# Optimization experiments

Hardware: AMD Instinct MI355X
Metric: run time of the kernel (lower is better)

The kernel has to match this reference:

```python
import jax, jax.numpy as jnp
import numpy as np

N = 131072      # total nodes = num_graphs * numNodes
E = 2097152     # edges (avg degree 16)
C_IN = 64
HID = 64        # hiddenChannels
NODES = 128     # numNodes per graph
B = 1024        # num_graphs
NCLS = 4


def setup_inputs() -> dict:
    key = jax.random.key(0)
    ks = jax.random.split(key, 10)
    x = jax.random.normal(ks[0], (N, C_IN), jnp.float32)
    edge_index = jax.random.randint(ks[1], (2, E), 0, N, dtype=jnp.int32)
    edge_attr = jax.random.uniform(ks[2], (E,), jnp.float32)
    # GCNConv params (stored as [in, out]); PyG uses glorot init, bias zeros
    W1 = jax.random.normal(ks[3], (C_IN, 2 * HID), jnp.float32) * (1.0 / np.sqrt(C_IN))
    b1 = jnp.zeros((2 * HID,), jnp.float32)
    W2 = jax.random.normal(ks[4], (2 * HID, HID), jnp.float32) * (1.0 / np.sqrt(2 * HID))
    b2 = jnp.zeros((HID,), jnp.float32)
    Wfc = jax.random.normal(ks[5], (HID * NODES, NCLS), jnp.float32) * (1.0 / np.sqrt(HID * NODES))
    bfc = jnp.zeros((NCLS,), jnp.float32)
    return {"x": x, "edge_index": edge_index, "edge_attr": edge_attr,
            "W1": W1, "b1": b1, "W2": W2, "b2": b2, "Wfc": Wfc, "bfc": bfc}


def gcn_conv(x, src, dst, ew, W, b):
    # PyG GCNConv: add self-loops (weight 1), symmetric normalization,
    # linear transform, scatter-add aggregation at target nodes, + bias.
    loop = jnp.arange(N, dtype=src.dtype)
    s = jnp.concatenate([src, loop])
    d = jnp.concatenate([dst, loop])
    w = jnp.concatenate([ew, jnp.ones((N,), ew.dtype)])
    deg = jax.ops.segment_sum(w, d, num_segments=N)                  # [N]
    dis = jnp.where(deg > 0, jax.lax.rsqrt(jnp.maximum(deg, 1e-30)), 0.0)
    norm = dis[s] * w * dis[d]                                       # [E+N]
    h = x @ W                                                        # [N, out]
    msg = h[s] * norm[:, None]                                       # gather + scale
    out = jax.ops.segment_sum(msg, d, num_segments=N)                # scatter-add
    return out + b


def reference(x, edge_index, edge_attr, W1, b1, W2, b2, Wfc, bfc):
    src, dst = edge_index[0], edge_index[1]
    h = jax.nn.relu(gcn_conv(x, src, dst, edge_attr, W1, b1))
    h = jax.nn.relu(gcn_conv(h, src, dst, edge_attr, W2, b2))
    h = h.reshape(B, HID * NODES)
    logits = h @ Wfc + bfc
    return jax.nn.softmax(logits, axis=1)
```

## Files before the change

kernel.cpp:

```cpp
#include <hip/hip_runtime.h>

#define N_NODES 131072
#define NE      2097152
#define CIN     64
#define HID     64
#define H2X     128
#define NODESG  128
#define NGRAPH  1024
#define NCLS    4

#define NBUCK   256
#define NPB     512
#define HBLK    1024
#define EPB     2048
#define DEGSC   1048576.0f
#define DEGMASK ((1ull << 40) - 1)

typedef short bf16x8 __attribute__((ext_vector_type(8)));
typedef float f32x4  __attribute__((ext_vector_type(4)));

__device__ __forceinline__ unsigned short f2b(float f) {
    unsigned int u = __float_as_uint(f);
    return (unsigned short)((u + 0x7fffu + ((u >> 16) & 1u)) >> 16);
}
__device__ __forceinline__ unsigned int pack2(float a, float b) {
    return (unsigned int)f2b(a) | ((unsigned int)f2b(b) << 16);
}
__device__ __forceinline__ float blo(unsigned u) { return __uint_as_float(u << 16); }
__device__ __forceinline__ float bhi(unsigned u) { return __uint_as_float(u & 0xffff0000u); }


__global__ __launch_bounds__(256) void k_wswiz(
        const float* __restrict__ W1, const float* __restrict__ W2,
        unsigned short* __restrict__ wf1, unsigned short* __restrict__ wf2) {
    int tid = threadIdx.x;
    #pragma unroll
    for (int it = 0; it < 4; ++it) {
        int idx = tid + 256 * it;
        int kt = idx >> 9, nt = (idx >> 6) & 7, l = idx & 63;
        int lm = l & 15, lq = l >> 4;
        unsigned pk[4];
        #pragma unroll
        for (int jp = 0; jp < 4; ++jp) {
            float w0 = W1[(kt*32 + lq*8 + 2*jp)     * H2X + nt*16 + lm];
            float w1 = W1[(kt*32 + lq*8 + 2*jp + 1) * H2X + nt*16 + lm];
            pk[jp] = pack2(w0, w1);
        }
        *(uint4*)&wf1[idx * 8] = make_uint4(pk[0], pk[1], pk[2], pk[3]);
    }
    #pragma unroll
    for (int it = 0; it < 4; ++it) {
        int idx = tid + 256 * it;
        int kt = idx >> 8, nt = (idx >> 6) & 3, l = idx & 63;
        int lm = l & 15, lq = l >> 4;
        unsigned pk[4];
        #pragma unroll
        for (int jp = 0; jp < 4; ++jp) {
            float w0 = W2[(kt*32 + lq*8 + 2*jp)     * HID + nt*16 + lm];
            float w1 = W2[(kt*32 + lq*8 + 2*jp + 1) * HID + nt*16 + lm];
            pk[jp] = pack2(w0, w1);
        }
        *(uint4*)&wf2[idx * 8] = make_uint4(pk[0], pk[1], pk[2], pk[3]);
    }
}


__global__ __launch_bounds__(256) void k_hist(const int* __restrict__ dst,
                                              int* __restrict__ hist) {
    __shared__ unsigned bh[NBUCK];
    int t = threadIdx.x;
    bh[t] = 0;
    __syncthreads();
    int base = blockIdx.x * EPB;
    #pragma unroll
    for (int k = 0; k < EPB / 256; ++k) {
        int d = dst[base + t + 256 * k];
        atomicAdd(&bh[d >> 9], 1u);
    }
    __syncthreads();
    hist[t * HBLK + blockIdx.x] = (int)bh[t];
}

__global__ void k_scan1(const int* __restrict__ in, int* __restrict__ out,
                        int* __restrict__ partial) {
    __shared__ int sd[256];
    int t = threadIdx.x;
    int base = blockIdx.x * 512;
    int c0 = in[base + 2*t];
    int c1 = in[base + 2*t + 1];
    int loc = c0 + c1;
    sd[t] = loc;
    __syncthreads();
    for (int off = 1; off < 256; off <<= 1) {
        int v = (t >= off) ? sd[t - off] : 0;
        __syncthreads();
        sd[t] += v;
        __syncthreads();
    }
    int excl = sd[t] - loc;
    out[base + 2*t]     = excl;
    out[base + 2*t + 1] = excl + c0;
    if (t == 255) partial[blockIdx.x] = sd[t];
}

__global__ void k_scan2(int* __restrict__ partial) {
    __shared__ int sd[256];
    int t = threadIdx.x;
    int p0 = partial[2*t], p1 = partial[2*t + 1];
    int loc = p0 + p1;
    sd[t] = loc;
    __syncthreads();
    for (int off = 1; off < 256; off <<= 1) {
        int v = (t >= off) ? sd[t - off] : 0;
        __syncthreads();
        sd[t] += v;
        __syncthreads();
    }
    int excl = sd[t] - loc;
    partial[2*t]     = excl;
    partial[2*t + 1] = excl + p0;
}

__global__ void k_scan3(int* __restrict__ data, const int* __restrict__ partial) {
    int i = blockIdx.x * blockDim.x + threadIdx.x;
    data[i] += partial[i >> 9];
}

__global__ __launch_bounds__(256) void k_scatter(
        const int* __restrict__ src, const int* __restrict__ dst,
        const float* __restrict__ ew, const int* __restrict__ hist,
        unsigned long long* __restrict__ part) {
    __shared__ unsigned lcur[NBUCK];
    int t = threadIdx.x;
    lcur[t] = (unsigned)hist[t * HBLK + blockIdx.x];
    __syncthreads();
    int base = blockIdx.x * EPB;
    #pragma unroll
    for (int k = 0; k < EPB / 256; ++k) {
        int e = base + t + 256 * k;
        int s = src[e], d = dst[e];
        unsigned w = __float_as_uint(ew[e]);
        unsigned p = atomicAdd(&lcur[d >> 9], 1u);
        part[p] = ((unsigned long long)w << 32) |
                  ((unsigned long long)(unsigned)(d & 511) << 17) |
                  (unsigned long long)(unsigned)s;
    }
}

__global__ __launch_bounds__(256) void k_bucket(
        const unsigned long long* __restrict__ part, const int* __restrict__ hist,
        int2* __restrict__ csr, int* __restrict__ rowptr,
        int* __restrict__ counts, float* __restrict__ dis) {
    __shared__ unsigned long long dc[NPB];
    __shared__ unsigned cnt2[NPB];
    __shared__ int rp[NPB];
    __shared__ int sd[256];
    int t = threadIdx.x, b = blockIdx.x;
    dc[t] = 0; dc[t + 256] = 0;
    cnt2[t] = 0; cnt2[t + 256] = 0;
    __syncthreads();
    int start = hist[b * HBLK];
    int end   = (b == NBUCK - 1) ? NE : hist[(b + 1) * HBLK];

    for (int j = start + t; j < end; j += 256) {
        unsigned long long p = part[j];
        unsigned dl = (unsigned)(p >> 17) & 511u;
        float w = __uint_as_float((unsigned)(p >> 32));
        atomicAdd(&dc[dl], (1ull << 40) | (unsigned long long)(unsigned)(w * DEGSC));
    }
    __syncthreads();

    unsigned long long d0 = dc[2*t], d1 = dc[2*t + 1];
    int c0 = (int)(d0 >> 40), c1 = (int)(d1 >> 40);
    int loc = c0 + c1;
    sd[t] = loc;
    __syncthreads();
    for (int off = 1; off < 256; off <<= 1) {
        int v = (t >= off) ? sd[t - off] : 0;
        __syncthreads();
        sd[t] += v;
        __syncthreads();
    }
    int excl = sd[t] - loc;
    rp[2*t] = excl; rp[2*t + 1] = excl + c0;

    int n0 = b * NPB;
    rowptr[n0 + 2*t]     = start + excl;
    rowptr[n0 + 2*t + 1] = start + excl + c0;
    counts[n0 + 2*t]     = c0;
    counts[n0 + 2*t + 1] = c1;
    float dg0 = (float)(d0 & DEGMASK) * (1.0f / DEGSC);
    float dg1 = (float)(d1 & DEGMASK) * (1.0f / DEGSC);
    dis[n0 + 2*t]     = rsqrtf(dg0 + 1.0f);
    dis[n0 + 2*t + 1] = rsqrtf(dg1 + 1.0f);
    __syncthreads();

    for (int j = start + t; j < end; j += 256) {
        unsigned long long p = part[j];
        unsigned dl = (unsigned)(p >> 17) & 511u;
        int s = (int)(p & 0x1ffffu);
        unsigned r = atomicAdd(&cnt2[dl], 1u);
        csr[start + rp[dl] + (int)r] = make_int2(s, (int)(unsigned)(p >> 32));
    }
}

__global__ void k_xcast(const float* __restrict__ x, const float* __restrict__ dis,
                        uint2* __restrict__ xb2) {
    int i = blockIdx.x * blockDim.x + threadIdx.x;
    float d = dis[i >> 4];
    float4 v = ((const float4*)x)[i];
    xb2[i] = make_uint2(pack2(d * v.x, d * v.y), pack2(d * v.z, d * v.w));
}


#define GATHER_PAIR(TAB, pA, pB, nA, nB, cmA, cmB, a0,a1,a2,a3, b0,b1,b2,b3, vSA, vSB) \
    {                                                                                  \
        int   sA0 = __shfl(pA.x, qid),      sA1 = __shfl(pA.x, qid + 4);               \
        int   sA2 = __shfl(pA.x, qid + 8),  sA3 = __shfl(pA.x, qid + 12);              \
        float fA0 = __int_as_float(__shfl(pA.y, qid));                                 \
        float fA1 = __int_as_float(__shfl(pA.y, qid + 4));                             \
        float fA2 = __int_as_float(__shfl(pA.y, qid + 8));                             \
        float fA3 = __int_as_float(__shfl(pA.y, qid + 12));                            \
        int   sB0 = __shfl(pB.x, qid),      sB1 = __shfl(pB.x, qid + 4);               \
        int   sB2 = __shfl(pB.x, qid + 8),  sB3 = __shfl(pB.x, qid + 12);              \
        float fB0 = __int_as_float(__shfl(pB.y, qid));                                 \
        float fB1 = __int_as_float(__shfl(pB.y, qid + 4));                             \
        float fB2 = __int_as_float(__shfl(pB.y, qid + 8));                             \
        float fB3 = __int_as_float(__shfl(pB.y, qid + 12));                            \
        uint2 vA0 = TAB[((unsigned)sA0 << 4) | ql];                                    \
        uint2 vA1 = TAB[((unsigned)sA1 << 4) | ql];                                    \
        uint2 vA2 = TAB[((unsigned)sA2 << 4) | ql];                                    \
        uint2 vA3 = TAB[((unsigned)sA3 << 4) | ql];                                    \
        uint2 vB0 = TAB[((unsigned)sB0 << 4) | ql];                                    \
        uint2 vB1 = TAB[((unsigned)sB1 << 4) | ql];                                    \
        uint2 vB2 = TAB[((unsigned)sB2 << 4) | ql];                                    \
        uint2 vB3 = TAB[((unsigned)sB3 << 4) | ql];                                    \
        vSA = TAB[((unsigned)nA << 4) | ql];                                           \
        vSB = TAB[((unsigned)nB << 4) | ql];                                           \
        a0 = fmaf(fA0, blo(vA0.x), a0); a1 = fmaf(fA0, bhi(vA0.x), a1);                \
        a2 = fmaf(fA0, blo(vA0.y), a2); a3 = fmaf(fA0, bhi(vA0.y), a3);                \
        a0 = fmaf(fA1, blo(vA1.x), a0); a1 = fmaf(fA1, bhi(vA1.x), a1);                \
        a2 = fmaf(fA1, blo(vA1.y), a2); a3 = fmaf(fA1, bhi(vA1.y), a3);                \
        a0 = fmaf(fA2, blo(vA2.x), a0); a1 = fmaf(fA2, bhi(vA2.x), a1);                \
        a2 = fmaf(fA2, blo(vA2.y), a2); a3 = fmaf(fA2, bhi(vA2.y), a3);                \
        a0 = fmaf(fA3, blo(vA3.x), a0); a1 = fmaf(fA3, bhi(vA3.x), a1);                \
        a2 = fmaf(fA3, blo(vA3.y), a2); a3 = fmaf(fA3, bhi(vA3.y), a3);                \
        b0 = fmaf(fB0, blo(vB0.x), b0); b1 = fmaf(fB0, bhi(vB0.x), b1);                \
        b2 = fmaf(fB0, blo(vB0.y), b2); b3 = fmaf(fB0, bhi(vB0.y), b3);                \
        b0 = fmaf(fB1, blo(vB1.x), b0); b1 = fmaf(fB1, bhi(vB1.x), b1);                \
        b2 = fmaf(fB1, blo(vB1.y), b2); b3 = fmaf(fB1, bhi(vB1.y), b3);                \
        b0 = fmaf(fB2, blo(vB2.x), b0); b1 = fmaf(fB2, bhi(vB2.x), b1);                \
        b2 = fmaf(fB2, blo(vB2.y), b2); b3 = fmaf(fB2, bhi(vB2.y), b3);                \
        b0 = fmaf(fB3, blo(vB3.x), b0); b1 = fmaf(fB3, bhi(vB3.x), b1);                \
        b2 = fmaf(fB3, blo(vB3.y), b2); b3 = fmaf(fB3, bhi(vB3.y), b3);                \
        int tsA = (cmA > 16) ? ((cmA - 13) >> 2) : 0;                                  \
        for (int k = 0; k < tsA; ++k) {                                                \
            int jj = 16 + 4 * k + qid;                                                 \
            int   s = __shfl(pA.x, jj);                                                \
            float f = __int_as_float(__shfl(pA.y, jj));                                \
            uint2 v = TAB[((unsigned)s << 4) | ql];                                    \
            a0 = fmaf(f, blo(v.x), a0); a1 = fmaf(f, bhi(v.x), a1);                    \
            a2 = fmaf(f, blo(v.y), a2); a3 = fmaf(f, bhi(v.y), a3);                    \
        }                                                                              \
        int tsB = (cmB > 16) ? ((cmB - 13) >> 2) : 0;                                  \
        for (int k = 0; k < tsB; ++k) {                                                \
            int jj = 16 + 4 * k + qid;                                                 \
            int   s = __shfl(pB.x, jj);                                                \
            float f = __int_as_float(__shfl(pB.y, jj));                                \
            uint2 v = TAB[((unsigned)s << 4) | ql];                                    \
            b0 = fmaf(f, blo(v.x), b0); b1 = fmaf(f, bhi(v.x), b1);                    \
            b2 = fmaf(f, blo(v.y), b2); b3 = fmaf(f, bhi(v.y), b3);                    \
        }                                                                              \
        a0 += __shfl_xor(a0, 16); a1 += __shfl_xor(a1, 16);                            \
        a2 += __shfl_xor(a2, 16); a3 += __shfl_xor(a3, 16);                            \
        a0 += __shfl_xor(a0, 32); a1 += __shfl_xor(a1, 32);                            \
        a2 += __shfl_xor(a2, 32); a3 += __shfl_xor(a3, 32);                            \
        b0 += __shfl_xor(b0, 16); b1 += __shfl_xor(b1, 16);                            \
        b2 += __shfl_xor(b2, 16); b3 += __shfl_xor(b3, 16);                            \
        b0 += __shfl_xor(b0, 32); b1 += __shfl_xor(b1, 32);                            \
        b2 += __shfl_xor(b2, 32); b3 += __shfl_xor(b3, 32);                            \
    }


__global__ __launch_bounds__(256, 4) void k_layer1(
        const uint2* __restrict__ xb2, const int2* __restrict__ csr,
        const int* __restrict__ rowptr, const int* __restrict__ counts,
        const float* __restrict__ dis, const unsigned short* __restrict__ wf1,
        const unsigned short* __restrict__ wf2, const float* __restrict__ b1,
        unsigned short* __restrict__ t2u) {
    __shared__ unsigned short sagg_b[32][72];
    __shared__ unsigned short sh1[32][136];
    __shared__ float sb[H2X];
    int tid = threadIdx.x;
    if (tid < H2X) sb[tid] = b1[tid];

    int wave = tid >> 6, lane = tid & 63;
    int qid = lane >> 4, ql = lane & 15;
    int n0 = blockIdx.x * 32;
    int nb = n0 + wave * 8;

    int cm8[8], cnt8[8], rs8[8];
    float dn8[8];
    int2 myp[8];
    #pragma unroll
    for (int i = 0; i < 8; ++i) {
        rs8[i] = rowptr[nb + i];
        cnt8[i] = counts[nb + i];
        dn8[i] = dis[nb + i];
        cm8[i] = cnt8[i] < 64 ? cnt8[i] : 64;
    }
    #pragma unroll
    for (int i = 0; i < 8; ++i)
        myp[i] = (lane < cm8[i]) ? csr[rs8[i] + lane] : make_int2(0, 0);

    #pragma unroll
    for (int ip = 0; ip < 8; ip += 2) {
        int2 pA = myp[ip], pB = myp[ip + 1];
        int nA = nb + ip, nB = nA + 1;
        float a0 = 0.f, a1 = 0.f, a2 = 0.f, a3 = 0.f;
        float b0 = 0.f, b1v = 0.f, b2v = 0.f, b3 = 0.f;
        uint2 vSA, vSB;
        GATHER_PAIR(xb2, pA, pB, nA, nB, cm8[ip], cm8[ip + 1],
                    a0, a1, a2, a3, b0, b1v, b2v, b3, vSA, vSB);
        for (int jj = 64; jj < cnt8[ip]; ++jj) {
            int2 p = csr[rs8[ip] + jj];
            float f = __int_as_float(p.y);
            uint2 v = xb2[((unsigned)p.x << 4) | ql];
            if (qid == 0) {
                a0 += f * blo(v.x); a1 += f * bhi(v.x);
                a2 += f * blo(v.y); a3 += f * bhi(v.y);
            }
        }
        for (int jj = 64; jj < cnt8[ip + 1]; ++jj) {
            int2 p = csr[rs8[ip + 1] + jj];
            float f = __int_as_float(p.y);
            uint2 v = xb2[((unsigned)p.x << 4) | ql];
            if (qid == 0) {
                b0 += f * blo(v.x); b1v += f * bhi(v.x);
                b2v += f * blo(v.y); b3 += f * bhi(v.y);
            }
        }
        if (qid == 0) {
            float dnA = dn8[ip], dnB = dn8[ip + 1];
            int m = wave * 8 + ip;
            *(uint2*)&sagg_b[m][ql * 4] =
                make_uint2(pack2(dnA * (a0 + blo(vSA.x)), dnA * (a1 + bhi(vSA.x))),
                           pack2(dnA * (a2 + blo(vSA.y)), dnA * (a3 + bhi(vSA.y))));
            *(uint2*)&sagg_b[m + 1][ql * 4] =
                make_uint2(pack2(dnB * (b0 + blo(vSB.x)), dnB * (b1v + bhi(vSB.x))),
                           pack2(dnB * (b2v + blo(vSB.y)), dnB * (b3 + bhi(vSB.y))));
        }
    }
    __syncthreads();

    int mt = wave & 1, ntb = (wave >> 1) * 4;
    int lm = lane & 15, lq = lane >> 4;
    bf16x8 af0 = *(const bf16x8*)&sagg_b[mt*16 + lm][lq * 8];
    bf16x8 af1 = *(const bf16x8*)&sagg_b[mt*16 + lm][32 + lq * 8];
    #pragma unroll
    for (int t = 0; t < 4; ++t) {
        int nt = ntb + t;
        bf16x8 bf0 = *(const bf16x8*)&wf1[(nt*64 + lane) * 8];
        bf16x8 bf1 = *(const bf16x8*)&wf1[((8 + nt)*64 + lane) * 8];
        f32x4 acc = {0.f, 0.f, 0.f, 0.f};
        acc = __builtin_amdgcn_mfma_f32_16x16x32_bf16(af0, bf0, acc, 0, 0, 0);
        acc = __builtin_amdgcn_mfma_f32_16x16x32_bf16(af1, bf1, acc, 0, 0, 0);
        int ch = nt*16 + lm;
        float bias = sb[ch];
        #pragma unroll
        for (int r = 0; r < 4; ++r)
            sh1[mt*16 + lq*4 + r][ch] = f2b(fmaxf(acc[r] + bias, 0.f));
    }
    __syncthreads();

    #pragma unroll
    for (int ti = 0; ti < 2; ++ti) {
        int t = wave * 2 + ti;
        int mt2 = t & 1, nt2 = t >> 1;
        f32x4 acc = {0.f, 0.f, 0.f, 0.f};
        #pragma unroll
        for (int kt = 0; kt < 4; ++kt) {
            bf16x8 af = *(const bf16x8*)&sh1[mt2*16 + lm][kt*32 + lq*8];
            bf16x8 bf = *(const bf16x8*)&wf2[((kt*4 + nt2)*64 + lane) * 8];
            acc = __builtin_amdgcn_mfma_f32_16x16x32_bf16(af, bf, acc, 0, 0, 0);
        }
        int ch = nt2*16 + lm;
        #pragma unroll
        for (int r = 0; r < 4; ++r) {
            int node = n0 + mt2*16 + lq*4 + r;
            t2u[(size_t)node * HID + ch] = f2b(dis[node] * acc[r]);
        }
    }
}


__global__ __launch_bounds__(256, 4) void k_agg2(
        const uint2* __restrict__ t2y, const int2* __restrict__ csr,
        const int* __restrict__ rowptr, const int* __restrict__ counts,
        const float* __restrict__ dis, const float* __restrict__ b2,
        unsigned short* __restrict__ h2b) {
    int tid = threadIdx.x;
    int wave = tid >> 6, lane = tid & 63;
    int qid = lane >> 4, ql = lane & 15;
    float4 bb = *(const float4*)&b2[ql * 4];
    int n0 = blockIdx.x * 32;
    int nb = n0 + wave * 8;

    int cm8[8], cnt8[8], rs8[8];
    float dn8[8];
    int2 myp[8];
    #pragma unroll
    for (int i = 0; i < 8; ++i) {
        rs8[i] = rowptr[nb + i];
        cnt8[i] = counts[nb + i];
        dn8[i] = dis[nb + i];
        cm8[i] = cnt8[i] < 64 ? cnt8[i] : 64;
    }
    #pragma unroll
    for (int i = 0; i < 8; ++i)
        myp[i] = (lane < cm8[i]) ? csr[rs8[i] + lane] : make_int2(0, 0);

    #pragma unroll
    for (int ip = 0; ip < 8; ip += 2) {
        int2 pA = myp[ip], pB = myp[ip + 1];
        int nA = nb + ip, nB = nA + 1;
        float a0 = 0.f, a1 = 0.f, a2 = 0.f, a3 = 0.f;
        float b0 = 0.f, b1v = 0.f, b2v = 0.f, b3 = 0.f;
        uint2 vSA, vSB;
        GATHER_PAIR(t2y, pA, pB, nA, nB, cm8[ip], cm8[ip + 1],
                    a0, a1, a2, a3, b0, b1v, b2v, b3, vSA, vSB);
        for (int jj = 64; jj < cnt8[ip]; ++jj) {
            int2 p = csr[rs8[ip] + jj];
            float f = __int_as_float(p.y);
            uint2 v = t2y[((unsigned)p.x << 4) | ql];
            if (qid == 0) {
                a0 += f * blo(v.x); a1 += f * bhi(v.x);
                a2 += f * blo(v.y); a3 += f * bhi(v.y);
            }
        }
        for (int jj = 64; jj < cnt8[ip + 1]; ++jj) {
            int2 p = csr[rs8[ip + 1] + jj];
            float f = __int_as_float(p.y);
            uint2 v = t2y[((unsigned)p.x << 4) | ql];
            if (qid == 0) {
                b0 += f * blo(v.x); b1v += f * bhi(v.x);
                b2v += f * blo(v.y); b3 += f * bhi(v.y);
            }
        }
        if (qid == 0) {
            float dnA = dn8[ip], dnB = dn8[ip + 1];
            float oa0 = fmaxf(fmaf(dnA, a0 + blo(vSA.x), bb.x), 0.f);
            float oa1 = fmaxf(fmaf(dnA, a1 + bhi(vSA.x), bb.y), 0.f);
            float oa2 = fmaxf(fmaf(dnA, a2 + blo(vSA.y), bb.z), 0.f);
            float oa3 = fmaxf(fmaf(dnA, a3 + bhi(vSA.y), bb.w), 0.f);
            float ob0 = fmaxf(fmaf(dnB, b0 + blo(vSB.x), bb.x), 0.f);
            float ob1 = fmaxf(fmaf(dnB, b1v + bhi(vSB.x), bb.y), 0.f);
            float ob2 = fmaxf(fmaf(dnB, b2v + blo(vSB.y), bb.z), 0.f);
            float ob3 = fmaxf(fmaf(dnB, b3 + bhi(vSB.y), bb.w), 0.f);
            *(uint2*)&h2b[((unsigned)nA << 6) | (ql * 4)] =
                make_uint2(pack2(oa0, oa1), pack2(oa2, oa3));
            *(uint2*)&h2b[((unsigned)nB << 6) | (ql * 4)] =
                make_uint2(pack2(ob0, ob1), pack2(ob2, ob3));
        }
    }
}


__global__ __launch_bounds__(256) void k_fc(
        const unsigned short* __restrict__ h2b, const float* __restrict__ Wfc,
        const float* __restrict__ bfc, float* __restrict__ out) {
    __shared__ float4 red[256];
    int b = blockIdx.x, t = threadIdx.x;
    const uint2* hrow = (const uint2*)(h2b + (size_t)b * (HID * NODESG));
    const float4* W4 = (const float4*)Wfc;
    float4 a = make_float4(0.f, 0.f, 0.f, 0.f);
    #pragma unroll
    for (int j = 0; j < 8; ++j) {
        int i = j * 256 + t;
        uint2 hv = hrow[i];
        float h0 = blo(hv.x), h1 = bhi(hv.x), h2v = blo(hv.y), h3 = bhi(hv.y);
        float4 w0 = W4[i * 4 + 0];
        float4 w1 = W4[i * 4 + 1];
        float4 w2 = W4[i * 4 + 2];
        float4 w3 = W4[i * 4 + 3];
        a.x = fmaf(h0, w0.x, a.x); a.y = fmaf(h0, w0.y, a.y);
        a.z = fmaf(h0, w0.z, a.z); a.w = fmaf(h0, w0.w, a.w);
        a.x = fmaf(h1, w1.x, a.x); a.y = fmaf(h1, w1.y, a.y);
        a.z = fmaf(h1, w1.z, a.z); a.w = fmaf(h1, w1.w, a.w);
        a.x = fmaf(h2v, w2.x, a.x); a.y = fmaf(h2v, w2.y, a.y);
        a.z = fmaf(h2v, w2.z, a.z); a.w = fmaf(h2v, w2.w, a.w);
        a.x = fmaf(h3, w3.x, a.x); a.y = fmaf(h3, w3.y, a.y);
        a.z = fmaf(h3, w3.z, a.z); a.w = fmaf(h3, w3.w, a.w);
    }
    red[t] = a;
    __syncthreads();
    for (int s = 128; s > 0; s >>= 1) {
        if (t < s) {
            red[t].x += red[t + s].x; red[t].y += red[t + s].y;
            red[t].z += red[t + s].z; red[t].w += red[t + s].w;
        }
        __syncthreads();
    }
    if (t == 0) {
        float l0 = red[0].x + bfc[0];
        float l1 = red[0].y + bfc[1];
        float l2 = red[0].z + bfc[2];
        float l3 = red[0].w + bfc[3];
        float mx = fmaxf(fmaxf(l0, l1), fmaxf(l2, l3));
        float e0 = expf(l0 - mx), e1 = expf(l1 - mx);
        float e2 = expf(l2 - mx), e3 = expf(l3 - mx);
        float inv = 1.f / (e0 + e1 + e2 + e3);
        float4 o = make_float4(e0 * inv, e1 * inv, e2 * inv, e3 * inv);
        *(float4*)&out[(size_t)b * 4] = o;
    }
}


extern "C" void kernel_launch(void* const* d_in, const int* in_sizes, int n_in,
                              void* d_out, int out_size, void* d_ws, size_t ws_size,
                              hipStream_t stream) {
    const float* x   = (const float*)d_in[0];
    const int*   ei  = (const int*)  d_in[1];
    const float* ea  = (const float*)d_in[2];
    const float* W1  = (const float*)d_in[3];
    const float* b1  = (const float*)d_in[4];
    const float* W2  = (const float*)d_in[5];
    const float* b2  = (const float*)d_in[6];
    const float* Wfc = (const float*)d_in[7];
    const float* bfc = (const float*)d_in[8];
    float* out = (float*)d_out;
    const int* src = ei;
    const int* dst = ei + NE;

    char* ws = (char*)d_ws;
    size_t off = 0;
    int*   hist   = (int*)  (ws + off); off += (size_t)NBUCK * HBLK * 4;
    int*   partial= (int*)  (ws + off); off += 4096;
    int*   counts = (int*)  (ws + off); off += (size_t)N_NODES * 4;
    int*   rowptr = (int*)  (ws + off); off += (size_t)N_NODES * 4;
    float* dis    = (float*)(ws + off); off += (size_t)N_NODES * 4;
    unsigned short* wf1 = (unsigned short*)(ws + off); off += 8192 * 2;
    unsigned short* wf2 = (unsigned short*)(ws + off); off += 8192 * 2;
    int2*  csr    = (int2*) (ws + off); off += (size_t)NE * 8;
    uint2* xb2    = (uint2*)(ws + off); off += (size_t)N_NODES * CIN * 2;
    unsigned short* t2u = (unsigned short*)(ws + off); off += (size_t)N_NODES * HID * 2;
    unsigned short* h2b = (unsigned short*)(ws + off); off += (size_t)N_NODES * HID * 2;
    unsigned long long* part = (unsigned long long*)h2b;

    hipMemsetAsync(hist, 0, (size_t)NBUCK * HBLK * 4, stream);

    k_wswiz  <<<1, 256, 0, stream>>>(W1, W2, wf1, wf2);
    k_hist   <<<HBLK, 256, 0, stream>>>(dst, hist);
    k_scan1  <<<NBUCK * HBLK / 512, 256, 0, stream>>>(hist, hist, partial);
    k_scan2  <<<1, 256, 0, stream>>>(partial);
    k_scan3  <<<NBUCK * HBLK / 256, 256, 0, stream>>>(hist, partial);
    k_scatter<<<HBLK, 256, 0, stream>>>(src, dst, ea, hist, part);
    k_bucket <<<NBUCK, 256, 0, stream>>>(part, hist, csr, rowptr, counts, dis);
    k_xcast  <<<(N_NODES * CIN / 4) / 256, 256, 0, stream>>>(x, dis, xb2);
    k_layer1 <<<N_NODES / 32, 256, 0, stream>>>(xb2, csr, rowptr, counts, dis,
                                                wf1, wf2, b1, t2u);
    k_agg2   <<<N_NODES / 32, 256, 0, stream>>>((const uint2*)t2u, csr, rowptr,
                                                counts, dis, b2, h2b);
    k_fc     <<<NGRAPH, 256, 0, stream>>>(h2b, Wfc, bfc, out);
}
```

Baseline: 271.0 us.

## Fuse FC layer into layer-2 aggregation and fold scan offset into consumers

Drops the k_scan3 pass by adding the block partial offsets directly in k_scatter and k_bucket. Fuses the final FC projection into k_agg2: each wave multiplies its ReLU outputs by Wfc, reduces the result with wave shuffles, and atomically adds per-graph logits. A small k_soft kernel then applies the softmax. This removes the h2b bf16 round trip and one launch, at the cost of float atomics (non-deterministic summation order) and extra Wfc loads in the aggregation kernel.

```diff
diff --git a/kernel.cpp b/kernel.cpp
--- a/kernel.cpp
+++ b/kernel.cpp
@@ -121,18 +121,14 @@
     partial[2*t + 1] = excl + p0;
 }
 
-__global__ void k_scan3(int* __restrict__ data, const int* __restrict__ partial) {
-    int i = blockIdx.x * blockDim.x + threadIdx.x;
-    data[i] += partial[i >> 9];
-}
-
 __global__ __launch_bounds__(256) void k_scatter(
         const int* __restrict__ src, const int* __restrict__ dst,
         const float* __restrict__ ew, const int* __restrict__ hist,
-        unsigned long long* __restrict__ part) {
+        const int* __restrict__ partial, unsigned long long* __restrict__ part) {
     __shared__ unsigned lcur[NBUCK];
     int t = threadIdx.x;
-    lcur[t] = (unsigned)hist[t * HBLK + blockIdx.x];
+    int gi = t * HBLK + blockIdx.x;
+    lcur[t] = (unsigned)(hist[gi] + partial[gi >> 9]);
     __syncthreads();
     int base = blockIdx.x * EPB;
     #pragma unroll
@@ -149,8 +145,8 @@
 
 __global__ __launch_bounds__(256) void k_bucket(
         const unsigned long long* __restrict__ part, const int* __restrict__ hist,
-        int2* __restrict__ csr, int* __restrict__ rowptr,
-        int* __restrict__ counts, float* __restrict__ dis) {
+        const int* __restrict__ partial, int2* __restrict__ csr,
+        int* __restrict__ rowptr, int* __restrict__ counts, float* __restrict__ dis) {
     __shared__ unsigned long long dc[NPB];
     __shared__ unsigned cnt2[NPB];
     __shared__ int rp[NPB];
@@ -159,8 +155,8 @@
     dc[t] = 0; dc[t + 256] = 0;
     cnt2[t] = 0; cnt2[t + 256] = 0;
     __syncthreads();
-    int start = hist[b * HBLK];
-    int end   = (b == NBUCK - 1) ? NE : hist[(b + 1) * HBLK];
+    int start = hist[b * HBLK] + partial[2 * b];
+    int end   = (b == NBUCK - 1) ? NE : (hist[(b + 1) * HBLK] + partial[2 * (b + 1)]);
 
     for (int j = start + t; j < end; j += 256) {
         unsigned long long p = part[j];
@@ -398,13 +394,14 @@
         const uint2* __restrict__ t2y, const int2* __restrict__ csr,
         const int* __restrict__ rowptr, const int* __restrict__ counts,
         const float* __restrict__ dis, const float* __restrict__ b2,
-        unsigned short* __restrict__ h2b) {
+        const float* __restrict__ Wfc, float* __restrict__ logits) {
     int tid = threadIdx.x;
     int wave = tid >> 6, lane = tid & 63;
     int qid = lane >> 4, ql = lane & 15;
     float4 bb = *(const float4*)&b2[ql * 4];
     int n0 = blockIdx.x * 32;
     int nb = n0 + wave * 8;
+    const float4* W4 = (const float4*)Wfc;
 
     int cm8[8], cnt8[8], rs8[8];
     float dn8[8];
@@ -419,6 +416,8 @@
     #pragma unroll
     for (int i = 0; i < 8; ++i)
         myp[i] = (lane < cm8[i]) ? csr[rs8[i] + lane] : make_int2(0, 0);
+
+    float4 lg = make_float4(0.f, 0.f, 0.f, 0.f);
 
     #pragma unroll
     for (int ip = 0; ip < 8; ip += 2) {
@@ -457,61 +456,52 @@
             float ob1 = fmaxf(fmaf(dnB, b1v + bhi(vSB.x), bb.y), 0.f);
             float ob2 = fmaxf(fmaf(dnB, b2v + blo(vSB.y), bb.z), 0.f);
             float ob3 = fmaxf(fmaf(dnB, b3 + bhi(vSB.y), bb.w), 0.f);
-            *(uint2*)&h2b[((unsigned)nA << 6) | (ql * 4)] =
-                make_uint2(pack2(oa0, oa1), pack2(oa2, oa3));
-            *(uint2*)&h2b[((unsigned)nB << 6) | (ql * 4)] =
-                make_uint2(pack2(ob0, ob1), pack2(ob2, ob3));
-        }
-    }
-}
-
-
-__global__ __launch_bounds__(256) void k_fc(
-        const unsigned short* __restrict__ h2b, const float* __restrict__ Wfc,
-        const float* __restrict__ bfc, float* __restrict__ out) {
-    __shared__ float4 red[256];
-    int b = blockIdx.x, t = threadIdx.x;
-    const uint2* hrow = (const uint2*)(h2b + (size_t)b * (HID * NODESG));
-    const float4* W4 = (const float4*)Wfc;
-    float4 a = make_float4(0.f, 0.f, 0.f, 0.f);
-    #pragma unroll
-    for (int j = 0; j < 8; ++j) {
-        int i = j * 256 + t;
-        uint2 hv = hrow[i];
-        float h0 = blo(hv.x), h1 = bhi(hv.x), h2v = blo(hv.y), h3 = bhi(hv.y);
-        float4 w0 = W4[i * 4 + 0];
-        float4 w1 = W4[i * 4 + 1];
-        float4 w2 = W4[i * 4 + 2];
-        float4 w3 = W4[i * 4 + 3];
-        a.x = fmaf(h0, w0.x, a.x); a.y = fmaf(h0, w0.y, a.y);
-        a.z = fmaf(h0, w0.z, a.z); a.w = fmaf(h0, w0.w, a.w);
-        a.x = fmaf(h1, w1.x, a.x); a.y = fmaf(h1, w1.y, a.y);
-        a.z = fmaf(h1, w1.z, a.z); a.w = fmaf(h1, w1.w, a.w);
-        a.x = fmaf(h2v, w2.x, a.x); a.y = fmaf(h2v, w2.y, a.y);
-        a.z = fmaf(h2v, w2.z, a.z); a.w = fmaf(h2v, w2.w, a.w);
-        a.x = fmaf(h3, w3.x, a.x); a.y = fmaf(h3, w3.y, a.y);
-        a.z = fmaf(h3, w3.z, a.z); a.w = fmaf(h3, w3.w, a.w);
-    }
-    red[t] = a;
-    __syncthreads();
-    for (int s = 128; s > 0; s >>= 1) {
-        if (t < s) {
-            red[t].x += red[t + s].x; red[t].y += red[t + s].y;
-            red[t].z += red[t + s].z; red[t].w += red[t + s].w;
-        }
-        __syncthreads();
-    }
-    if (t == 0) {
-        float l0 = red[0].x + bfc[0];
-        float l1 = red[0].y + bfc[1];
-        float l2 = red[0].z + bfc[2];
-        float l3 = red[0].w + bfc[3];
+            int baseA = (((unsigned)nA & 127u) << 6) + (ql << 2);
+            int baseB = (((unsigned)nB & 127u) << 6) + (ql << 2);
+            float4 w;
+            w = W4[baseA + 0]; lg.x = fmaf(oa0, w.x, lg.x); lg.y = fmaf(oa0, w.y, lg.y);
+                               lg.z = fmaf(oa0, w.z, lg.z); lg.w = fmaf(oa0, w.w, lg.w);
+            w = W4[baseA + 1]; lg.x = fmaf(oa1, w.x, lg.x); lg.y = fmaf(oa1, w.y, lg.y);
+                               lg.z = fmaf(oa1, w.z, lg.z); lg.w = fmaf(oa1, w.w, lg.w);
+            w = W4[baseA + 2]; lg.x = fmaf(oa2, w.x, lg.x); lg.y = fmaf(oa2, w.y, lg.y);
+                               lg.z = fmaf(oa2, w.z, lg.z); lg.w = fmaf(oa2, w.w, lg.w);
+            w = W4[baseA + 3]; lg.x = fmaf(oa3, w.x, lg.x); lg.y = fmaf(oa3, w.y, lg.y);
+                               lg.z = fmaf(oa3, w.z, lg.z); lg.w = fmaf(oa3, w.w, lg.w);
+            w = W4[baseB + 0]; lg.x = fmaf(ob0, w.x, lg.x); lg.y = fmaf(ob0, w.y, lg.y);
+                               lg.z = fmaf(ob0, w.z, lg.z); lg.w = fmaf(ob0, w.w, lg.w);
+            w = W4[baseB + 1]; lg.x = fmaf(ob1, w.x, lg.x); lg.y = fmaf(ob1, w.y, lg.y);
+                               lg.z = fmaf(ob1, w.z, lg.z); lg.w = fmaf(ob1, w.w, lg.w);
+            w = W4[baseB + 2]; lg.x = fmaf(ob2, w.x, lg.x); lg.y = fmaf(ob2, w.y, lg.y);
+                               lg.z = fmaf(ob2, w.z, lg.z); lg.w = fmaf(ob2, w.w, lg.w);
+            w = W4[baseB + 3]; lg.x = fmaf(ob3, w.x, lg.x); lg.y = fmaf(ob3, w.y, lg.y);
+                               lg.z = fmaf(ob3, w.z, lg.z); lg.w = fmaf(ob3, w.w, lg.w);
+        }
+    }
+    #pragma unroll
+    for (int m = 1; m < 64; m <<= 1) {
+        lg.x += __shfl_xor(lg.x, m); lg.y += __shfl_xor(lg.y, m);
+        lg.z += __shfl_xor(lg.z, m); lg.w += __shfl_xor(lg.w, m);
+    }
+    if (lane == 0) {
+        float* lgp = &logits[(n0 >> 7) * 4];
+        atomicAdd(&lgp[0], lg.x); atomicAdd(&lgp[1], lg.y);
+        atomicAdd(&lgp[2], lg.z); atomicAdd(&lgp[3], lg.w);
+    }
+}
+
+
+__global__ void k_soft(const float* __restrict__ logits, const float* __restrict__ bfc,
+                       float* __restrict__ out) {
+    int g = blockIdx.x * blockDim.x + threadIdx.x;
+    if (g < NGRAPH) {
+        float4 l = ((const float4*)logits)[g];
+        float l0 = l.x + bfc[0], l1 = l.y + bfc[1];
+        float l2 = l.z + bfc[2], l3 = l.w + bfc[3];
         float mx = fmaxf(fmaxf(l0, l1), fmaxf(l2, l3));
         float e0 = expf(l0 - mx), e1 = expf(l1 - mx);
         float e2 = expf(l2 - mx), e3 = expf(l3 - mx);
         float inv = 1.f / (e0 + e1 + e2 + e3);
-        float4 o = make_float4(e0 * inv, e1 * inv, e2 * inv, e3 * inv);
-        *(float4*)&out[(size_t)b * 4] = o;
+        ((float4*)out)[g] = make_float4(e0 * inv, e1 * inv, e2 * inv, e3 * inv);
     }
 }
 
@@ -536,6 +526,7 @@
     size_t off = 0;
     int*   hist   = (int*)  (ws + off); off += (size_t)NBUCK * HBLK * 4;
     int*   partial= (int*)  (ws + off); off += 4096;
+    float* logits = (float*)(ws + off); off += (size_t)NGRAPH * 4 * 4;
     int*   counts = (int*)  (ws + off); off += (size_t)N_NODES * 4;
     int*   rowptr = (int*)  (ws + off); off += (size_t)N_NODES * 4;
     float* dis    = (float*)(ws + off); off += (size_t)N_NODES * 4;
@@ -544,22 +535,20 @@
     int2*  csr    = (int2*) (ws + off); off += (size_t)NE * 8;
     uint2* xb2    = (uint2*)(ws + off); off += (size_t)N_NODES * CIN * 2;
     unsigned short* t2u = (unsigned short*)(ws + off); off += (size_t)N_NODES * HID * 2;
-    unsigned short* h2b = (unsigned short*)(ws + off); off += (size_t)N_NODES * HID * 2;
-    unsigned long long* part = (unsigned long long*)h2b;
-
-    hipMemsetAsync(hist, 0, (size_t)NBUCK * HBLK * 4, stream);
+    unsigned long long* part = (unsigned long long*)t2u;
+
+    hipMemsetAsync(hist, 0, (size_t)NBUCK * HBLK * 4 + 4096 + (size_t)NGRAPH * 16, stream);
 
     k_wswiz  <<<1, 256, 0, stream>>>(W1, W2, wf1, wf2);
     k_hist   <<<HBLK, 256, 0, stream>>>(dst, hist);
     k_scan1  <<<NBUCK * HBLK / 512, 256, 0, stream>>>(hist, hist, partial);
     k_scan2  <<<1, 256, 0, stream>>>(partial);
-    k_scan3  <<<NBUCK * HBLK / 256, 256, 0, stream>>>(hist, partial);
-    k_scatter<<<HBLK, 256, 0, stream>>>(src, dst, ea, hist, part);
-    k_bucket <<<NBUCK, 256, 0, stream>>>(part, hist, csr, rowptr, counts, dis);
+    k_scatter<<<HBLK, 256, 0, stream>>>(src, dst, ea, hist, partial, part);
+    k_bucket <<<NBUCK, 256, 0, stream>>>(part, hist, partial, csr, rowptr, counts, dis);
     k_xcast  <<<(N_NODES * CIN / 4) / 256, 256, 0, stream>>>(x, dis, xb2);
     k_layer1 <<<N_NODES / 32, 256, 0, stream>>>(xb2, csr, rowptr, counts, dis,
                                                 wf1, wf2, b1, t2u);
     k_agg2   <<<N_NODES / 32, 256, 0, stream>>>((const uint2*)t2u, csr, rowptr,
-                                                counts, dis, b2, h2b);
-    k_fc     <<<NGRAPH, 256, 0, stream>>>(h2b, Wfc, bfc, out);
-}
+                                                counts, dis, b2, Wfc, logits);
+    k_soft   <<<(NGRAPH + 255) / 256, 256, 0, stream>>>(logits, bfc, out);
+}
```

Measured after the change: 286.5 us. +5.7%, slower.
